# Optimization experiments

Measured on AMD Instinct MI355X. Metric: run time of the kernel, lower is better.

The kernel has to match this reference:

```python
import jax, jax.numpy as jnp
import numpy as np

B, S, E = 2, 2048, 1024
H = 16
D = E // H  # head_dim = 64
SCALE = D ** -0.5


def _rope_cos_sin(seq_len, dim, dtype=jnp.float32):
    inv_freq = 1.0 / (10000.0 ** (jnp.arange(0, dim, 2, dtype=jnp.float32) / dim))
    pos = jnp.arange(seq_len, dtype=jnp.float32)
    freqs = pos[:, None] * inv_freq[None, :]  # [S, D/2]
    return jnp.cos(freqs).astype(dtype), jnp.sin(freqs).astype(dtype)


def _apply_rope(x, cos, sin):
    # x: [B, H, S, D]; interleaved complex rotation on (even, odd) pairs
    x2 = x.reshape(*x.shape[:-1], D // 2, 2)
    xr, xi = x2[..., 0], x2[..., 1]
    c = cos[None, None, :, :]
    s = sin[None, None, :, :]
    out_r = xr * c - xi * s
    out_i = xr * s + xi * c
    return jnp.stack([out_r, out_i], axis=-1).reshape(x.shape)


def setup_inputs() -> dict:
    key = jax.random.key(0)
    k1, k2, k3, k4, k5 = jax.random.split(key, 5)
    query = jax.random.normal(k1, (B, S, E), dtype=jnp.float32)
    key_t = jax.random.normal(k2, (B, S, E), dtype=jnp.float32)
    value = jax.random.normal(k3, (B, S, E), dtype=jnp.float32)
    w_qkv = jax.random.normal(k4, (3 * E, E), dtype=jnp.float32) * 0.02
    w_out = jax.random.normal(k5, (E, E), dtype=jnp.float32) * 0.02
    return {"query": query, "key": key_t, "value": value,
            "w_qkv": w_qkv, "w_out": w_out}


def reference(query, key, value, w_qkv, w_out):
    # Fused QKV projection from query only (matches original module)
    qkv = jnp.einsum('bse,fe->bsf', query, w_qkv)  # [B, S, 3E]
    q, k, v = jnp.split(qkv, 3, axis=-1)
    to_heads = lambda t: t.reshape(B, S, H, D).transpose(0, 2, 1, 3)  # [B,H,S,D]
    q, k, v = to_heads(q), to_heads(k), to_heads(v)

    cos, sin = _rope_cos_sin(S, D, q.dtype)
    q = _apply_rope(q, cos, sin)
    k = _apply_rope(k, cos, sin)

    # Standard scaled dot-product attention (eval mode, no mask, no dropout)
    attn = jnp.einsum('bhsd,bhtd->bhst', q, k) * SCALE
    attn = jax.nn.softmax(attn.astype(jnp.float32), axis=-1).astype(q.dtype)
    ctx = jnp.einsum('bhst,bhtd->bhsd', attn, v)  # [B,H,S,D]

    out = ctx.transpose(0, 2, 1, 3).reshape(B, S, E)
    return jnp.einsum('bse,fe->bsf', out, w_out)
```

## Files before the change

### kernel.cpp

```cpp
#include <hip/hip_runtime.h>
#include <math.h>

typedef __attribute__((ext_vector_type(8))) __bf16 bf16x8;
typedef __attribute__((ext_vector_type(4))) __bf16 bf16x4;
typedef __attribute__((ext_vector_type(4))) float f32x4;

constexpr int kBATCH = 2;
constexpr int kS = 2048;
constexpr int kE = 1024;
constexpr int kH = 16;
constexpr int kD = 64;
constexpr float kScale = 0.125f;
constexpr float kQScale = 0.125f * 1.44269504088896340736f;

__device__ inline void gl2lds16(const void* g, void* l) {
    __builtin_amdgcn_global_load_lds((const __attribute__((address_space(1))) void*)g,
                                     (__attribute__((address_space(3))) void*)l, 16, 0, 0);
}

__global__ __launch_bounds__(256) void cvt2_kernel(const float* __restrict__ a, __bf16* __restrict__ oa, int na,
                                                   const float* __restrict__ b, __bf16* __restrict__ ob) {
    int idx = (blockIdx.x * 256 + threadIdx.x) * 4;
    const float* src;
    __bf16* dst;
    if (idx < na) { src = a + idx; dst = oa + idx; }
    else          { src = b + (idx - na); dst = ob + (idx - na); }
    float4 f = *(const float4*)src;
    bf16x4 r;
    r[0] = (__bf16)f.x; r[1] = (__bf16)f.y; r[2] = (__bf16)f.z; r[3] = (__bf16)f.w;
    *(bf16x4*)dst = r;
}

template <int TN, typename TC>
__global__ __launch_bounds__(256) void gemm_bt_kernel(const __bf16* __restrict__ A,
                                                      const __bf16* __restrict__ W,
                                                      TC* __restrict__ C,
                                                      int M, int N, int K) {
    constexpr int NI = TN / 32;
    __shared__ __bf16 As[128 * 64] __attribute__((aligned(16)));
    __shared__ __bf16 Bs[TN * 64] __attribute__((aligned(16)));

    const int tid  = threadIdx.x;
    const int lane = tid & 63;
    const int quad = lane >> 4;
    const int l16  = lane & 15;
    const int rx   = l16 & 7;
    const int wave = tid >> 6;
    const int wm   = (wave >> 1) * 64;
    const int wn   = (wave & 1) * (TN / 2);
    const int m0   = blockIdx.y * 128;
    const int n0   = blockIdx.x * TN;

    const int srow8  = lane >> 3;
    const int schunk = ((lane & 7) ^ srow8) * 8;

    f32x4 zero = {0.f, 0.f, 0.f, 0.f};
    f32x4 acc[4][NI];
#pragma unroll
    for (int i = 0; i < 4; ++i)
#pragma unroll
        for (int j = 0; j < NI; ++j) acc[i][j] = zero;

    for (int kt = 0; kt < K; kt += 64) {
        __syncthreads();
#pragma unroll
        for (int i = 0; i < 4; ++i) {
            int rbase = wave * 32 + i * 8;
            gl2lds16(A + (size_t)(m0 + rbase + srow8) * K + kt + schunk, &As[rbase * 64]);
        }
#pragma unroll
        for (int i = 0; i < NI; ++i) {
            int rbase = wave * (TN / 4) + i * 8;
            gl2lds16(W + (size_t)(n0 + rbase + srow8) * K + kt + schunk, &Bs[rbase * 64]);
        }
        __syncthreads();

#pragma unroll
        for (int kk = 0; kk < 2; ++kk) {
            bf16x8 af[4], bf[NI];
#pragma unroll
            for (int mi = 0; mi < 4; ++mi)
                af[mi] = *(const bf16x8*)(&As[(wm + mi * 16 + l16) * 64 + (((kk * 4 + quad) ^ rx)) * 8]);
#pragma unroll
            for (int ni = 0; ni < NI; ++ni)
                bf[ni] = *(const bf16x8*)(&Bs[(wn + ni * 16 + l16) * 64 + (((kk * 4 + quad) ^ rx)) * 8]);
#pragma unroll
            for (int mi = 0; mi < 4; ++mi)
#pragma unroll
                for (int ni = 0; ni < NI; ++ni)
                    acc[mi][ni] = __builtin_amdgcn_mfma_f32_16x16x32_bf16(af[mi], bf[ni], acc[mi][ni], 0, 0, 0);
        }
    }

#pragma unroll
    for (int mi = 0; mi < 4; ++mi)
#pragma unroll
        for (int ni = 0; ni < NI; ++ni)
#pragma unroll
            for (int r = 0; r < 4; ++r) {
                int row = m0 + wm + mi * 16 + quad * 4 + r;
                int col = n0 + wn + ni * 16 + l16;
                C[(size_t)row * N + col] = (TC)acc[mi][ni][r];
            }
}

__global__ __launch_bounds__(256) void rope_vtrans_kernel(const __bf16* __restrict__ qkv,
                                                          __bf16* __restrict__ qd,
                                                          __bf16* __restrict__ kd,
                                                          __bf16* __restrict__ vt) {
    __shared__ __bf16 tile[64 * 72] __attribute__((aligned(16)));

    if (blockIdx.x < 8192) {
        int tid = blockIdx.x * 256 + threadIdx.x;
        int i = tid & 31;
        int h = (tid >> 5) & (kH - 1);
        int s = (tid >> 9) & (kS - 1);
        int b = tid >> 20;

        size_t rowbase = (size_t)(b * kS + s) * (3 * kE);
        int coff = h * kD + 2 * i;

        float qr = (float)qkv[rowbase + coff];
        float qi = (float)qkv[rowbase + coff + 1];
        float kr = (float)qkv[rowbase + kE + coff];
        float ki = (float)qkv[rowbase + kE + coff + 1];

        float inv = expf(-(float)i * (9.210340371976184f / 32.0f));
        float ang = (float)s * inv;
        float cv = cosf(ang);
        float sv = sinf(ang);

        size_t qbase = ((size_t)(b * kH + h) * kS + s) * kD + 2 * i;
        qd[qbase]     = (__bf16)(kQScale * (qr * cv - qi * sv));
        qd[qbase + 1] = (__bf16)(kQScale * (qr * sv + qi * cv));
        kd[qbase]     = (__bf16)(kr * cv - ki * sv);
        kd[qbase + 1] = (__bf16)(kr * sv + ki * cv);
    } else {
        int flat = blockIdx.x - 8192;
        int s0 = (flat & 31) * 64;
        int bh = flat >> 5;
        int b = bh >> 4, h = bh & 15;
        int tid = threadIdx.x;

#pragma unroll
        for (int p = 0; p < 2; ++p) {
            int c = tid + p * 256;
            int r = c >> 3, jc = c & 7;
            *(bf16x8*)&tile[r * 72 + jc * 8] =
                *(const bf16x8*)(qkv + (size_t)(b * kS + s0 + r) * (3 * kE) + 2 * kE + h * kD + jc * 8);
        }
        __syncthreads();
#pragma unroll
        for (int p = 0; p < 2; ++p) {
            int c = tid + p * 256;
            int d = c >> 3, jt = c & 7;
            bf16x8 v;
#pragma unroll
            for (int u = 0; u < 8; ++u) {
                int src = (jt >> 2) * 32 + ((u >> 2) << 4) + ((jt & 3) << 2) + (u & 3);
                v[u] = tile[src * 72 + d];
            }
            *(bf16x8*)(vt + (size_t)(bh * kD + d) * kS + s0 + jt * 8) = v;
        }
    }
}

__global__ __launch_bounds__(256, 2) void attn_kernel(const __bf16* __restrict__ qd,
                                                      const __bf16* __restrict__ kd,
                                                      const __bf16* __restrict__ vt,
                                                      __bf16* __restrict__ ctx,
                                                      const float* __restrict__ wout,
                                                      __bf16* __restrict__ woutb) {
    __shared__ __bf16 Ks[2][64 * 64] __attribute__((aligned(16)));
    __shared__ __bf16 Vs[4][64 * 64] __attribute__((aligned(16)));

    const int lane = threadIdx.x & 63;
    const int wave = threadIdx.x >> 6;
    const int quad = lane >> 4;
    const int l16  = lane & 15;
    const int rx   = l16 & 7;

    {
        int base = blockIdx.x * 2048 + threadIdx.x * 8;
#pragma unroll
        for (int p = 0; p < 2; ++p) {
            float4 f = *(const float4*)(wout + base + p * 4);
            bf16x4 r;
            r[0] = (__bf16)f.x; r[1] = (__bf16)f.y; r[2] = (__bf16)f.z; r[3] = (__bf16)f.w;
            *(bf16x4*)(woutb + base + p * 4) = r;
        }
    }

    const int flat = blockIdx.x;
    const int s    = flat >> 3;
    const int bh   = (flat & 7) * 4 + (s >> 4);
    const int q0   = (s & 15) * 128;
    const int b  = bh >> 4;
    const int h  = bh & 15;

    const __bf16* qp = qd + (size_t)bh * kS * kD;
    const __bf16* kp = kd + (size_t)bh * kS * kD;
    const __bf16* vp = vt + (size_t)bh * kD * kS;

    const int srow8  = lane >> 3;
    const int schunk = ((lane & 7) ^ srow8) * 8;

    bf16x8 aq[2][2];
#pragma unroll
    for (int qg = 0; qg < 2; ++qg) {
        const __bf16* qrow = qp + (size_t)(q0 + wave * 32 + qg * 16 + l16) * kD + quad * 8;
        aq[qg][0] = *(const bf16x8*)(qrow);
        aq[qg][1] = *(const bf16x8*)(qrow + 32);
    }

    bf16x8 vone;
#pragma unroll
    for (int u = 0; u < 8; ++u) vone[u] = (__bf16)1.0f;

    f32x4 zero = {0.f, 0.f, 0.f, 0.f};
    f32x4 acc[2][4];
    f32x4 asum[2] = {zero, zero};
#pragma unroll
    for (int qg = 0; qg < 2; ++qg)
#pragma unroll
        for (int i = 0; i < 4; ++i) acc[qg][i] = zero;

    f32x4 sgb[2][2][4];

    int koff[4][2], voff[4][2];
#pragma unroll
    for (int g = 0; g < 4; ++g) {
        int row = g * 16 + l16;
        koff[g][0] = row * 64 + ((quad       ^ rx)) * 8;
        koff[g][1] = row * 64 + (((quad + 4) ^ rx)) * 8;
        voff[g][0] = row * 64 + ((quad       ^ (row & 7))) * 8;
        voff[g][1] = row * 64 + (((quad + 4) ^ (row & 7))) * 8;
    }

    const __bf16* kst[2];
    const __bf16* vst[2];
#pragma unroll
    for (int c = 0; c < 2; ++c) {
        int i = wave * 2 + c;
        kst[c] = kp + (size_t)(i * 8 + srow8) * kD + schunk;
        vst[c] = vp + (size_t)(i * 8 + srow8) * kS + schunk;
    }

    auto stage = [&](int ks, int vs) __attribute__((always_inline)) -> void {
#pragma unroll
        for (int c = 0; c < 2; ++c) {
            gl2lds16(kst[c], &Ks[ks][(wave * 2 + c) * 512]);
            gl2lds16(vst[c], &Vs[vs][(wave * 2 + c) * 512]);
            kst[c] += 64 * kD;
            vst[c] += 64;
        }
    };

    auto qk = [&](int kbuf, int par) __attribute__((always_inline)) -> void {
#pragma unroll
        for (int g = 0; g < 4; ++g) {
            bf16x8 a0 = *(const bf16x8*)&Ks[kbuf][koff[g][0]];
            bf16x8 a1 = *(const bf16x8*)&Ks[kbuf][koff[g][1]];
#pragma unroll
            for (int qg = 0; qg < 2; ++qg) {
                f32x4 t = __builtin_amdgcn_mfma_f32_16x16x32_bf16(a0, aq[qg][0], zero, 0, 0, 0);
                sgb[par][qg][g] = __builtin_amdgcn_mfma_f32_16x16x32_bf16(a1, aq[qg][1], t, 0, 0, 0);
            }
        }
    };

    auto expand = [&](bf16x8 (&ap)[2][2], int par) __attribute__((always_inline)) -> void {
#pragma unroll
        for (int qg = 0; qg < 2; ++qg)
#pragma unroll
            for (int r = 0; r < 4; ++r) {
                ap[qg][0][r]     = (__bf16)__builtin_amdgcn_exp2f(sgb[par][qg][0][r]);
                ap[qg][0][4 + r] = (__bf16)__builtin_amdgcn_exp2f(sgb[par][qg][1][r]);
                ap[qg][1][r]     = (__bf16)__builtin_amdgcn_exp2f(sgb[par][qg][2][r]);
                ap[qg][1][4 + r] = (__bf16)__builtin_amdgcn_exp2f(sgb[par][qg][3][r]);
            }
    };

    auto sumpv = [&](int vbuf, bf16x8 (&ap)[2][2]) __attribute__((always_inline)) -> void {
#pragma unroll
        for (int qg = 0; qg < 2; ++qg) {
            asum[qg] = __builtin_amdgcn_mfma_f32_16x16x32_bf16(ap[qg][0], vone, asum[qg], 0, 0, 0);
            asum[qg] = __builtin_amdgcn_mfma_f32_16x16x32_bf16(ap[qg][1], vone, asum[qg], 0, 0, 0);
        }
#pragma unroll
        for (int nt = 0; nt < 4; ++nt) {
            bf16x8 bv0 = *(const bf16x8*)&Vs[vbuf][voff[nt][0]];
            bf16x8 bv1 = *(const bf16x8*)&Vs[vbuf][voff[nt][1]];
#pragma unroll
            for (int qg = 0; qg < 2; ++qg) {
                acc[qg][nt] = __builtin_amdgcn_mfma_f32_16x16x32_bf16(ap[qg][0], bv0, acc[qg][nt], 0, 0, 0);
                acc[qg][nt] = __builtin_amdgcn_mfma_f32_16x16x32_bf16(ap[qg][1], bv1, acc[qg][nt], 0, 0, 0);
            }
        }
    };

    auto body = [&](int kbuf, int vprev, int vnext, bool pf, int pin)
        __attribute__((always_inline)) -> void {
        __syncthreads();
        if (pf) stage(kbuf ^ 1, vnext);
        bf16x8 ap[2][2];
        expand(ap, pin);
        __builtin_amdgcn_s_setprio(1);
        qk(kbuf, pin ^ 1);
        sumpv(vprev, ap);
        __builtin_amdgcn_s_setprio(0);
    };

    stage(0, 0);
    __syncthreads();
    stage(1, 1);
    __builtin_amdgcn_s_setprio(1);
    qk(0, 0);
    __builtin_amdgcn_s_setprio(0);

#pragma unroll 1
    for (int t0 = 1; t0 < 29; t0 += 4) {
        body(1, 0, 2, true, 0);
        body(0, 1, 3, true, 1);
        body(1, 2, 0, true, 0);
        body(0, 3, 1, true, 1);
    }
    body(1, 0, 2, true, 0);
    body(0, 1, 3, true, 1);
    body(1, 2, 0, false, 0);

    {
        bf16x8 ap[2][2];
        expand(ap, 1);
        sumpv(3, ap);
    }

#pragma unroll
    for (int qg = 0; qg < 2; ++qg)
#pragma unroll
        for (int r = 0; r < 4; ++r) {
            float inv_l = 1.0f / asum[qg][r];
            int srow_q = q0 + wave * 32 + qg * 16 + quad * 4 + r;
#pragma unroll
            for (int nt = 0; nt < 4; ++nt) {
                int col = h * kD + nt * 16 + l16;
                ctx[(size_t)(b * kS + srow_q) * kE + col] = (__bf16)(acc[qg][nt][r] * inv_l);
            }
        }
}

extern "C" void kernel_launch(void* const* d_in, const int* in_sizes, int n_in,
                              void* d_out, int out_size, void* d_ws, size_t ws_size,
                              hipStream_t stream) {
    const float* query = (const float*)d_in[0];
    const float* w_qkv = (const float*)d_in[3];
    const float* w_out = (const float*)d_in[4];
    float* out = (float*)d_out;

    const int M = kBATCH * kS;
    const int nQ = M * kE;
    const int nWqkv = 3 * kE * kE;

    char* ws = (char*)d_ws;
    __bf16* qkv_raw = (__bf16*)ws;
    __bf16* ctx     = (__bf16*)ws;
    __bf16* w_out_b = (__bf16*)(ws + (size_t)8388608);
    __bf16* qd      = (__bf16*)(ws + (size_t)25165824);
    __bf16* kd      = (__bf16*)(ws + (size_t)33554432);
    __bf16* vt      = (__bf16*)(ws + (size_t)41943040);
    __bf16* query_b = qd;
    __bf16* w_qkv_b = kd;

    cvt2_kernel<<<(nQ + nWqkv) / 1024, 256, 0, stream>>>(query, query_b, nQ, w_qkv, w_qkv_b);

    gemm_bt_kernel<128, __bf16>
        <<<dim3(3 * kE / 128, M / 128), 256, 0, stream>>>(query_b, w_qkv_b, qkv_raw, M, 3 * kE, kE);

    rope_vtrans_kernel<<<8192 + 1024, 256, 0, stream>>>(qkv_raw, qd, kd, vt);

    attn_kernel<<<512, 256, 0, stream>>>(qd, kd, vt, ctx, w_out, w_out_b);

    gemm_bt_kernel<64, float>
        <<<dim3(kE / 64, M / 128), 256, 0, stream>>>(ctx, w_out_b, out, M, kE, kE);
}
```

Before: 197.2 us.

## Fuse RoPE and Q scaling into QKV GEMM epilogue with precomputed cos/sin table

Adds a dedicated QKV GEMM whose epilogue applies RoPE (using a lane shuffle to pair even and odd columns) and writes Q and K directly in head-major layout. V is written to a compact buffer and transposed by a smaller standalone kernel. A cos/sin table is filled by extra blocks of the conversion kernel. This drops the separate RoPE pass and the full qkv intermediate round trip. In exchange the GEMM epilogue does scattered 2-byte stores and table loads.

```diff
diff --git a/kernel.cpp b/kernel.cpp
--- a/kernel.cpp
+++ b/kernel.cpp
@@ -19,7 +19,20 @@
 }
 
 __global__ __launch_bounds__(256) void cvt2_kernel(const float* __restrict__ a, __bf16* __restrict__ oa, int na,
-                                                   const float* __restrict__ b, __bf16* __restrict__ ob) {
+                                                   const float* __restrict__ b, __bf16* __restrict__ ob,
+                                                   float2* __restrict__ tab) {
+    if (blockIdx.x >= 7168) {
+        int e = (blockIdx.x - 7168) * 1024 + threadIdx.x * 4;
+#pragma unroll
+        for (int j = 0; j < 4; ++j) {
+            int ee = e + j;
+            int s = ee >> 5, i = ee & 31;
+            float inv = expf(-(float)i * (9.210340371976184f / 32.0f));
+            float ang = (float)s * inv;
+            tab[ee] = make_float2(cosf(ang), sinf(ang));
+        }
+        return;
+    }
     int idx = (blockIdx.x * 256 + threadIdx.x) * 4;
     const float* src;
     __bf16* dst;
@@ -29,6 +42,105 @@
     bf16x4 r;
     r[0] = (__bf16)f.x; r[1] = (__bf16)f.y; r[2] = (__bf16)f.z; r[3] = (__bf16)f.w;
     *(bf16x4*)dst = r;
+}
+
+__global__ __launch_bounds__(256) void gemm_qkv_kernel(const __bf16* __restrict__ A,
+                                                       const __bf16* __restrict__ W,
+                                                       __bf16* __restrict__ vraw,
+                                                       __bf16* __restrict__ qd,
+                                                       __bf16* __restrict__ kd,
+                                                       const float2* __restrict__ tab) {
+    constexpr int kK = 1024;
+    __shared__ __bf16 As[128 * 64] __attribute__((aligned(16)));
+    __shared__ __bf16 Bs[128 * 64] __attribute__((aligned(16)));
+
+    const int tid  = threadIdx.x;
+    const int lane = tid & 63;
+    const int quad = lane >> 4;
+    const int l16  = lane & 15;
+    const int rx   = l16 & 7;
+    const int wave = tid >> 6;
+    const int wm   = (wave >> 1) * 64;
+    const int wn   = (wave & 1) * 64;
+    const int m0   = blockIdx.y * 128;
+    const int n0   = blockIdx.x * 128;
+
+    const int srow8  = lane >> 3;
+    const int schunk = ((lane & 7) ^ srow8) * 8;
+
+    f32x4 zero = {0.f, 0.f, 0.f, 0.f};
+    f32x4 acc[4][4];
+#pragma unroll
+    for (int i = 0; i < 4; ++i)
+#pragma unroll
+        for (int j = 0; j < 4; ++j) acc[i][j] = zero;
+
+    for (int kt = 0; kt < kK; kt += 64) {
+        __syncthreads();
+#pragma unroll
+        for (int i = 0; i < 4; ++i) {
+            int rbase = wave * 32 + i * 8;
+            gl2lds16(A + (size_t)(m0 + rbase + srow8) * kK + kt + schunk, &As[rbase * 64]);
+            gl2lds16(W + (size_t)(n0 + rbase + srow8) * kK + kt + schunk, &Bs[rbase * 64]);
+        }
+        __syncthreads();
+
+#pragma unroll
+        for (int kk = 0; kk < 2; ++kk) {
+            bf16x8 af[4], bf[4];
+#pragma unroll
+            for (int mi = 0; mi < 4; ++mi)
+                af[mi] = *(const bf16x8*)(&As[(wm + mi * 16 + l16) * 64 + (((kk * 4 + quad) ^ rx)) * 8]);
+#pragma unroll
+            for (int ni = 0; ni < 4; ++ni)
+                bf[ni] = *(const bf16x8*)(&Bs[(wn + ni * 16 + l16) * 64 + (((kk * 4 + quad) ^ rx)) * 8]);
+#pragma unroll
+            for (int mi = 0; mi < 4; ++mi)
+#pragma unroll
+                for (int ni = 0; ni < 4; ++ni)
+                    acc[mi][ni] = __builtin_amdgcn_mfma_f32_16x16x32_bf16(af[mi], bf[ni], acc[mi][ni], 0, 0, 0);
+        }
+    }
+
+    const int col0 = n0 + wn;
+    const int reg  = col0 >> 10;
+    const int h    = (col0 >> 6) & 15;
+
+    if (reg == 2) {
+#pragma unroll
+        for (int mi = 0; mi < 4; ++mi)
+#pragma unroll
+            for (int ni = 0; ni < 4; ++ni)
+#pragma unroll
+                for (int r = 0; r < 4; ++r) {
+                    int row  = m0 + wm + mi * 16 + quad * 4 + r;
+                    int colv = col0 - 2048 + ni * 16 + l16;
+                    vraw[(size_t)row * kE + colv] = (__bf16)acc[mi][ni][r];
+                }
+    } else {
+        __bf16* dst = reg ? kd : qd;
+        const float qs = reg ? 1.0f : kQScale;
+        const bool odd = (l16 & 1);
+#pragma unroll
+        for (int mi = 0; mi < 4; ++mi)
+#pragma unroll
+            for (int r = 0; r < 4; ++r) {
+                int srow = m0 + wm + mi * 16 + quad * 4 + r;
+                int sloc = srow & (kS - 1);
+                int bb   = srow >> 11;
+                const float2* trow = tab + sloc * 32;
+                __bf16* drow = dst + ((size_t)(bb * kH + h) * kS + sloc) * kD;
+#pragma unroll
+                for (int ni = 0; ni < 4; ++ni) {
+                    int d = ni * 16 + l16;
+                    float2 cs = trow[d >> 1];
+                    float v  = acc[mi][ni][r];
+                    float pv = __shfl_xor(v, 1);
+                    float out = odd ? (pv * cs.y + v * cs.x) : (v * cs.x - pv * cs.y);
+                    drow[d] = (__bf16)(qs * out);
+                }
+            }
+    }
 }
 
 template <int TN, typename TC>
@@ -104,64 +216,35 @@
             }
 }
 
-__global__ __launch_bounds__(256) void rope_vtrans_kernel(const __bf16* __restrict__ qkv,
-                                                          __bf16* __restrict__ qd,
-                                                          __bf16* __restrict__ kd,
-                                                          __bf16* __restrict__ vt) {
+__global__ __launch_bounds__(256) void vtrans_kernel(const __bf16* __restrict__ vraw,
+                                                     __bf16* __restrict__ vt) {
     __shared__ __bf16 tile[64 * 72] __attribute__((aligned(16)));
 
-    if (blockIdx.x < 8192) {
-        int tid = blockIdx.x * 256 + threadIdx.x;
-        int i = tid & 31;
-        int h = (tid >> 5) & (kH - 1);
-        int s = (tid >> 9) & (kS - 1);
-        int b = tid >> 20;
-
-        size_t rowbase = (size_t)(b * kS + s) * (3 * kE);
-        int coff = h * kD + 2 * i;
-
-        float qr = (float)qkv[rowbase + coff];
-        float qi = (float)qkv[rowbase + coff + 1];
-        float kr = (float)qkv[rowbase + kE + coff];
-        float ki = (float)qkv[rowbase + kE + coff + 1];
-
-        float inv = expf(-(float)i * (9.210340371976184f / 32.0f));
-        float ang = (float)s * inv;
-        float cv = cosf(ang);
-        float sv = sinf(ang);
-
-        size_t qbase = ((size_t)(b * kH + h) * kS + s) * kD + 2 * i;
-        qd[qbase]     = (__bf16)(kQScale * (qr * cv - qi * sv));
-        qd[qbase + 1] = (__bf16)(kQScale * (qr * sv + qi * cv));
-        kd[qbase]     = (__bf16)(kr * cv - ki * sv);
-        kd[qbase + 1] = (__bf16)(kr * sv + ki * cv);
-    } else {
-        int flat = blockIdx.x - 8192;
-        int s0 = (flat & 31) * 64;
-        int bh = flat >> 5;
-        int b = bh >> 4, h = bh & 15;
-        int tid = threadIdx.x;
-
-#pragma unroll
-        for (int p = 0; p < 2; ++p) {
-            int c = tid + p * 256;
-            int r = c >> 3, jc = c & 7;
-            *(bf16x8*)&tile[r * 72 + jc * 8] =
-                *(const bf16x8*)(qkv + (size_t)(b * kS + s0 + r) * (3 * kE) + 2 * kE + h * kD + jc * 8);
-        }
-        __syncthreads();
-#pragma unroll
-        for (int p = 0; p < 2; ++p) {
-            int c = tid + p * 256;
-            int d = c >> 3, jt = c & 7;
-            bf16x8 v;
-#pragma unroll
-            for (int u = 0; u < 8; ++u) {
-                int src = (jt >> 2) * 32 + ((u >> 2) << 4) + ((jt & 3) << 2) + (u & 3);
-                v[u] = tile[src * 72 + d];
-            }
-            *(bf16x8*)(vt + (size_t)(bh * kD + d) * kS + s0 + jt * 8) = v;
-        }
+    int flat = blockIdx.x;
+    int s0 = (flat & 31) * 64;
+    int bh = flat >> 5;
+    int b = bh >> 4, h = bh & 15;
+    int tid = threadIdx.x;
+
+#pragma unroll
+    for (int p = 0; p < 2; ++p) {
+        int c = tid + p * 256;
+        int r = c >> 3, jc = c & 7;
+        *(bf16x8*)&tile[r * 72 + jc * 8] =
+            *(const bf16x8*)(vraw + (size_t)(b * kS + s0 + r) * kE + h * kD + jc * 8);
+    }
+    __syncthreads();
+#pragma unroll
+    for (int p = 0; p < 2; ++p) {
+        int c = tid + p * 256;
+        int d = c >> 3, jt = c & 7;
+        bf16x8 v;
+#pragma unroll
+        for (int u = 0; u < 8; ++u) {
+            int src = (jt >> 2) * 32 + ((u >> 2) << 4) + ((jt & 3) << 2) + (u & 3);
+            v[u] = tile[src * 72 + d];
+        }
+        *(bf16x8*)(vt + (size_t)(bh * kD + d) * kS + s0 + jt * 8) = v;
     }
 }
 
@@ -362,21 +445,22 @@
     const int nWqkv = 3 * kE * kE;
 
     char* ws = (char*)d_ws;
-    __bf16* qkv_raw = (__bf16*)ws;
+    __bf16* query_b = (__bf16*)ws;
+    __bf16* w_qkv_b = (__bf16*)(ws + ((size_t)8 << 20));
+    float2* tab     = (float2*)(ws + ((size_t)14 << 20));
+    __bf16* vraw    = (__bf16*)(ws + ((size_t)16 << 20));
+    __bf16* qd      = (__bf16*)(ws + ((size_t)24 << 20));
+    __bf16* kd      = (__bf16*)(ws + ((size_t)32 << 20));
+    __bf16* vt      = (__bf16*)(ws + ((size_t)40 << 20));
     __bf16* ctx     = (__bf16*)ws;
-    __bf16* w_out_b = (__bf16*)(ws + (size_t)8388608);
-    __bf16* qd      = (__bf16*)(ws + (size_t)25165824);
-    __bf16* kd      = (__bf16*)(ws + (size_t)33554432);
-    __bf16* vt      = (__bf16*)(ws + (size_t)41943040);
-    __bf16* query_b = qd;
-    __bf16* w_qkv_b = kd;
-
-    cvt2_kernel<<<(nQ + nWqkv) / 1024, 256, 0, stream>>>(query, query_b, nQ, w_qkv, w_qkv_b);
-
-    gemm_bt_kernel<128, __bf16>
-        <<<dim3(3 * kE / 128, M / 128), 256, 0, stream>>>(query_b, w_qkv_b, qkv_raw, M, 3 * kE, kE);
-
-    rope_vtrans_kernel<<<8192 + 1024, 256, 0, stream>>>(qkv_raw, qd, kd, vt);
+    __bf16* w_out_b = (__bf16*)(ws + ((size_t)8 << 20));
+
+    cvt2_kernel<<<7168 + 64, 256, 0, stream>>>(query, query_b, nQ, w_qkv, w_qkv_b, tab);
+
+    gemm_qkv_kernel<<<dim3(3 * kE / 128, M / 128), 256, 0, stream>>>(
+        query_b, w_qkv_b, vraw, qd, kd, tab);
+
+    vtrans_kernel<<<1024, 256, 0, stream>>>(vraw, vt);
 
     attn_kernel<<<512, 256, 0, stream>>>(qd, kd, vt, ctx, w_out, w_out_b);
 
```

After: 202.3 us. 2.6% more time.
